# Kernel optimization log

Measured on AMD Instinct MI355X. Metric: run time of the kernel, lower is better.

Reference implementation:

```python
import jax, jax.numpy as jnp
import numpy as np

D = 1024
H = 8
DK = D // H
BS, NSEG, NSEN = 16, 64, 32


def _linear_params(key, d_in, d_out, scale=0.02):
    kw, kb = jax.random.split(key)
    w = jax.random.normal(kw, (d_out, d_in), dtype=jnp.float32) * scale
    b = jax.random.normal(kb, (d_out,), dtype=jnp.float32) * scale
    return w, b


def setup_inputs() -> dict:
    key = jax.random.key(0)
    ks = jax.random.split(key, 12)
    A = jax.random.normal(ks[0], (BS, NSEG, D), dtype=jnp.float32)
    V = jax.random.normal(ks[1], (BS, NSEG, D), dtype=jnp.float32)
    S = jax.random.normal(ks[2], (BS, NSEN, D), dtype=jnp.float32)
    wA, bA = _linear_params(ks[3], D, D)
    wV, bV = _linear_params(ks[4], D, D)
    wS, bS = _linear_params(ks[5], D, D)
    wq, bq = _linear_params(ks[6], D, D)
    wk, bk = _linear_params(ks[7], D, D)
    wv, bv = _linear_params(ks[8], D, D)
    w1, b1 = _linear_params(ks[9], D, D)
    w2, b2 = _linear_params(ks[10], D, D)
    return {"A": A, "V": V, "S": S,
            "wA": wA, "bA": bA, "wV": wV, "bV": bV, "wS": wS, "bS": bS,
            "wq": wq, "bq": bq, "wk": wk, "bk": bk, "wv": wv, "bv": bv,
            "w1": w1, "b1": b1, "w2": w2, "b2": b2}


def _lin(x, w, b):
    return x @ w.T + b


def reference(A, V, S, wA, bA, wV, bV, wS, bS, wq, bq, wk, bk, wv, bv, w1, b1, w2, b2):
    bs, num_seg, d_model = A.shape
    num_sen = S.shape[1]
    A = _lin(A, wA, bA)
    V = _lin(V, wV, bV)
    S = _lin(S, wS, bS)
    av = jnp.stack([A, V], axis=2)                       # (bs, num_seg, 2, d)
    q = _lin(S, wq, bq).reshape(bs, num_sen, H, DK)      # (b, s, h, dk)
    k = _lin(av, wk, bk).reshape(bs, num_seg, 2, H, DK)  # (b, g, a, h, dk)
    v = _lin(av, wv, bv).reshape(bs, num_seg, 2, H, DK)
    # attention over the size-2 A/V axis only
    attn = jnp.einsum('bshd,bgahd->bsgah', q, k) / np.sqrt(DK).astype(np.float32)
    attn = jax.nn.softmax(attn, axis=3)                  # softmax over a (A vs V)
    out = jnp.einsum('bsgah,bgahd->bsghd', attn, v)
    out = out.reshape(bs, num_sen, num_seg, d_model)
    # positionwise FF: Linear -> ReLU -> Linear (dropout p=0)
    out = _lin(jax.nn.relu(_lin(out, w1, b1)), w2, b2)
    return out
```

## Files before the change

### kernel.cpp

```cpp
#include <hip/hip_runtime.h>
#include <stdint.h>


#define D_MODEL 1024
#define N_HEAD  8
#define DK      128
#define BS      16
#define NSEG    64
#define NSEN    32

typedef __attribute__((ext_vector_type(8))) __bf16 bf16x8;
typedef __attribute__((ext_vector_type(8))) unsigned short u16x8;
typedef __attribute__((ext_vector_type(4))) float f32x4;

__device__ __forceinline__ float bf2f(unsigned short b) {
  union { unsigned int u; float f; } x; x.u = ((unsigned int)b) << 16; return x.f;
}
__device__ __forceinline__ unsigned short f2bf(float f) {
  union { float f; unsigned int u; } x; x.f = f;
  unsigned int u = x.u;
  unsigned int r = (u + 0x7fffu + ((u >> 16) & 1u)) >> 16;
  return (unsigned short)r;
}

__device__ __forceinline__ void g2l16(const void* g, void* l) {
  __builtin_amdgcn_global_load_lds(
      (const __attribute__((address_space(1))) void*)g,
      (__attribute__((address_space(3))) void*)l, 16, 0, 0);
}

struct CvtB { const float* s[11]; unsigned short* d[11]; int n4[11]; };
__global__ __launch_bounds__(256)
void cvtall_kernel(CvtB p) {
  const int z = blockIdx.y;
  const int i = blockIdx.x * 256 + threadIdx.x;
  if (i >= p.n4[z]) return;
  float4 v = reinterpret_cast<const float4*>(p.s[z])[i];
  ushort4 o;
  o.x = f2bf(v.x); o.y = f2bf(v.y); o.z = f2bf(v.z); o.w = f2bf(v.w);
  reinterpret_cast<ushort4*>(p.d[z])[i] = o;
}

struct GSeg { const unsigned short* A; const unsigned short* B;
              const float* bias; unsigned short* C; };
struct GBatch { GSeg s[3]; int end[3]; };

__global__ __launch_bounds__(256)
void gemm64_bt(GBatch gb) {
  __shared__ __align__(16) unsigned short lA[2][64 * 32];
  __shared__ __align__(16) unsigned short lB[2][128 * 32];

  const int nwg = gridDim.x;
  const int sw = (blockIdx.x & 7) * (nwg >> 3) + (blockIdx.x >> 3);
  int sgi = 0, base = 0;
  if (sw >= gb.end[0]) { sgi = 1; base = gb.end[0]; }
  if (sw >= gb.end[1]) { sgi = 2; base = gb.end[1]; }
  const GSeg sg = gb.s[sgi];
  const int st = sw - base;
  const int m0 = (st >> 3) * 64, n0 = (st & 7) * 128;

  const int t = threadIdx.x;
  const int lane = t & 63, w = t >> 6;
  const int fr = lane & 15, kg = lane >> 4;

  f32x4 acc[2][4] = {};

  const int r  = t >> 2;
  const int c8 = (t & 3) * 8;
  const unsigned short* ga  = sg.A + (size_t)(m0 + r) * 1024 + c8;
  const unsigned short* gbp = sg.B + (size_t)(n0 + r) * 1024 + c8;

  auto stage = [&](int buf, int k0) {
    g2l16(ga + k0,              &lA[buf][t * 8]);
    g2l16(gbp + k0,             &lB[buf][t * 8]);
    g2l16(gbp + k0 + 64 * 1024, &lB[buf][2048 + t * 8]);
  };

  stage(0, 0);
  asm volatile("s_waitcnt vmcnt(0)" ::: "memory");
  __syncthreads();

  for (int k0 = 0; k0 < 1024; k0 += 32) {
    const int buf = (k0 >> 5) & 1;
    if (k0 + 32 < 1024) stage(buf ^ 1, k0 + 32);

    u16x8 af[4], bf[2];
#pragma unroll
    for (int mi = 0; mi < 4; ++mi)
      af[mi] = *reinterpret_cast<const u16x8*>(&lA[buf][(mi * 16 + fr) * 32 + kg * 8]);
#pragma unroll
    for (int ni = 0; ni < 2; ++ni)
      bf[ni] = *reinterpret_cast<const u16x8*>(&lB[buf][(w * 32 + ni * 16 + fr) * 32 + kg * 8]);
#pragma unroll
    for (int ni = 0; ni < 2; ++ni)
#pragma unroll
      for (int mi = 0; mi < 4; ++mi)
        acc[ni][mi] = __builtin_amdgcn_mfma_f32_16x16x32_bf16(
            __builtin_bit_cast(bf16x8, bf[ni]), __builtin_bit_cast(bf16x8, af[mi]),
            acc[ni][mi], 0, 0, 0);

    asm volatile("s_waitcnt vmcnt(0)" ::: "memory");
    __syncthreads();
  }

#pragma unroll
  for (int ni = 0; ni < 2; ++ni) {
    const int gn0 = n0 + w * 32 + ni * 16 + kg * 4;
    const float4 bv = *reinterpret_cast<const float4*>(&sg.bias[gn0]);
#pragma unroll
    for (int mi = 0; mi < 4; ++mi) {
      const int gm = m0 + mi * 16 + fr;
      ushort4 o;
      o.x = f2bf(acc[ni][mi][0] + bv.x);
      o.y = f2bf(acc[ni][mi][1] + bv.y);
      o.z = f2bf(acc[ni][mi][2] + bv.z);
      o.w = f2bf(acc[ni][mi][3] + bv.w);
      *reinterpret_cast<ushort4*>(&sg.C[(size_t)gm * 1024 + gn0]) = o;
    }
  }
}

__global__ __launch_bounds__(512, 2)
void gemm8p_bt(const unsigned short* __restrict__ A, const unsigned short* __restrict__ B,
               const float* __restrict__ bias, float* __restrict__ C,
               int M, int N, int K, int nbx) {
  __shared__ __align__(16) unsigned short lds[2][2][256][64];

  const int nwg = gridDim.x;
  const int sw = (blockIdx.x & 7) * (nwg >> 3) + (blockIdx.x >> 3);
  const int m0 = (sw / nbx) * 256, n0 = (sw % nbx) * 256;

  const int T = threadIdx.x;
  const int lane = T & 63, wave = T >> 6;
  const int wr = wave >> 2, wc = wave & 3;
  const int fr = lane & 15, kg = lane >> 4;
  const int NT = K >> 6;

  const int sgs = (T & 7) ^ ((T >> 3) & 7);
  int grA[2][2], grB[2][2];
#pragma unroll
  for (int mh = 0; mh < 2; ++mh)
#pragma unroll
    for (int c = 0; c < 2; ++c) {
      int l = mh * 128 + c * 64 + (T >> 3);
      grA[mh][c] = ((l >> 6) & 1) * 128 + (l >> 7) * 64 + (l & 63);
      grB[mh][c] = ((l >> 5) & 3) * 64  + (l >> 7) * 32 + (l & 31);
    }
  const unsigned short* Abase = A + (size_t)m0 * K + sgs * 8;
  const unsigned short* Bbase = B + (size_t)n0 * K + sgs * 8;
  char* ldsc = (char*)&lds[0][0][0][0];

  auto stageA = [&](int buf, int mh, int t) {
#pragma unroll
    for (int c = 0; c < 2; ++c)
      g2l16(Abase + (size_t)grA[mh][c] * K + t * 64,
            ldsc + ((size_t)buf * 65536) + (mh * 128 + c * 64) * 128 + T * 16);
  };
  auto stageB = [&](int buf, int nh, int t) {
#pragma unroll
    for (int c = 0; c < 2; ++c)
      g2l16(Bbase + (size_t)grB[nh][c] * K + t * 64,
            ldsc + ((size_t)buf * 65536) + 32768 + (nh * 128 + c * 64) * 128 + T * 16);
  };

  int koff[2];
#pragma unroll
  for (int kk = 0; kk < 2; ++kk) koff[kk] = ((kk * 4 + kg) ^ (fr & 7)) * 16;
  int lrA[8], lrB[4];
#pragma unroll
  for (int mi = 0; mi < 8; ++mi) lrA[mi] = ((mi >> 2) * 128 + wr * 64 + (mi & 3) * 16 + fr) * 128;
#pragma unroll
  for (int ni = 0; ni < 4; ++ni) lrB[ni] = ((ni >> 1) * 128 + wc * 32 + (ni & 1) * 16 + fr) * 128;

  auto rdA = [&](int buf, int mi, int kk) -> u16x8 {
    return *reinterpret_cast<const u16x8*>(ldsc + (size_t)buf * 65536 + lrA[mi] + koff[kk]);
  };
  auto rdB = [&](int buf, int ni, int kk) -> u16x8 {
    return *reinterpret_cast<const u16x8*>(ldsc + (size_t)buf * 65536 + 32768 + lrB[ni] + koff[kk]);
  };

  f32x4 acc[4][8] = {};

  stageA(0, 0, 0); stageB(0, 0, 0); stageA(0, 1, 0); stageB(0, 1, 0);
  if (NT > 1) { stageA(1, 0, 1); stageB(1, 0, 1); stageA(1, 1, 1); }
  asm volatile("s_waitcnt vmcnt(6)" ::: "memory");
  __builtin_amdgcn_s_barrier();

  u16x8 af0[4][2], af1[4][2], bf0[2][2], bf1[2][2];

  for (int t = 0; t < NT; ++t) {
    const int buf = t & 1;
    const bool st1 = (t + 1 < NT), st2 = (t + 2 < NT);

#pragma unroll
    for (int mi = 0; mi < 4; ++mi)
#pragma unroll
      for (int kk = 0; kk < 2; ++kk) af0[mi][kk] = rdA(buf, mi, kk);
#pragma unroll
    for (int ni = 0; ni < 2; ++ni)
#pragma unroll
      for (int kk = 0; kk < 2; ++kk) bf0[ni][kk] = rdB(buf, ni, kk);
    if (st1) stageB(buf ^ 1, 1, t + 1);
    __builtin_amdgcn_s_barrier();
    asm volatile("s_waitcnt lgkmcnt(0)" ::: "memory");
    __builtin_amdgcn_sched_barrier(0);
    __builtin_amdgcn_s_setprio(1);
#pragma unroll
    for (int ni = 0; ni < 2; ++ni)
#pragma unroll
      for (int mi = 0; mi < 4; ++mi)
#pragma unroll
        for (int kk = 0; kk < 2; ++kk)
          acc[ni][mi] = __builtin_amdgcn_mfma_f32_16x16x32_bf16(
              __builtin_bit_cast(bf16x8, bf0[ni][kk]), __builtin_bit_cast(bf16x8, af0[mi][kk]),
              acc[ni][mi], 0, 0, 0);
    __builtin_amdgcn_s_setprio(0);
    __builtin_amdgcn_s_barrier();

#pragma unroll
    for (int ni = 0; ni < 2; ++ni)
#pragma unroll
      for (int kk = 0; kk < 2; ++kk) bf1[ni][kk] = rdB(buf, ni + 2, kk);
    if (st2) stageA(buf, 0, t + 2);
    __builtin_amdgcn_s_barrier();
    asm volatile("s_waitcnt lgkmcnt(0)" ::: "memory");
    __builtin_amdgcn_sched_barrier(0);
    __builtin_amdgcn_s_setprio(1);
#pragma unroll
    for (int ni = 0; ni < 2; ++ni)
#pragma unroll
      for (int mi = 0; mi < 4; ++mi)
#pragma unroll
        for (int kk = 0; kk < 2; ++kk)
          acc[ni + 2][mi] = __builtin_amdgcn_mfma_f32_16x16x32_bf16(
              __builtin_bit_cast(bf16x8, bf1[ni][kk]), __builtin_bit_cast(bf16x8, af0[mi][kk]),
              acc[ni + 2][mi], 0, 0, 0);
    __builtin_amdgcn_s_setprio(0);
    __builtin_amdgcn_s_barrier();

#pragma unroll
    for (int mi = 0; mi < 4; ++mi)
#pragma unroll
      for (int kk = 0; kk < 2; ++kk) af1[mi][kk] = rdA(buf, mi + 4, kk);
    if (st2) stageB(buf, 0, t + 2);
    __builtin_amdgcn_s_barrier();
    asm volatile("s_waitcnt lgkmcnt(0)" ::: "memory");
    __builtin_amdgcn_sched_barrier(0);
    __builtin_amdgcn_s_setprio(1);
#pragma unroll
    for (int ni = 0; ni < 2; ++ni)
#pragma unroll
      for (int mi = 0; mi < 4; ++mi)
#pragma unroll
        for (int kk = 0; kk < 2; ++kk)
          acc[ni + 2][mi + 4] = __builtin_amdgcn_mfma_f32_16x16x32_bf16(
              __builtin_bit_cast(bf16x8, bf1[ni][kk]), __builtin_bit_cast(bf16x8, af1[mi][kk]),
              acc[ni + 2][mi + 4], 0, 0, 0);
    __builtin_amdgcn_s_setprio(0);
    __builtin_amdgcn_s_barrier();

    if (st2) stageA(buf, 1, t + 2);
    __builtin_amdgcn_s_barrier();
    __builtin_amdgcn_s_setprio(1);
#pragma unroll
    for (int ni = 0; ni < 2; ++ni)
#pragma unroll
      for (int mi = 0; mi < 4; ++mi)
#pragma unroll
        for (int kk = 0; kk < 2; ++kk)
          acc[ni][mi + 4] = __builtin_amdgcn_mfma_f32_16x16x32_bf16(
              __builtin_bit_cast(bf16x8, bf0[ni][kk]), __builtin_bit_cast(bf16x8, af1[mi][kk]),
              acc[ni][mi + 4], 0, 0, 0);
    __builtin_amdgcn_s_setprio(0);
    if (st2)       asm volatile("s_waitcnt vmcnt(6)" ::: "memory");
    else if (st1)  asm volatile("s_waitcnt vmcnt(0)" ::: "memory");
    __builtin_amdgcn_s_barrier();
  }

#pragma unroll
  for (int ni = 0; ni < 4; ++ni) {
    const int gn0 = n0 + wc * 64 + ni * 16 + kg * 4;
    const float4 bv = *reinterpret_cast<const float4*>(&bias[gn0]);
#pragma unroll
    for (int mi = 0; mi < 8; ++mi) {
      const int gm = m0 + wr * 128 + mi * 16 + fr;
      float4 o;
      o.x = acc[ni][mi][0] + bv.x;
      o.y = acc[ni][mi][1] + bv.y;
      o.z = acc[ni][mi][2] + bv.z;
      o.w = acc[ni][mi][3] + bv.w;
      *reinterpret_cast<float4*>(&C[(size_t)gm * N + gn0]) = o;
    }
  }
}

__global__ __launch_bounds__(256)
void uav_gemm(const unsigned short* __restrict__ vAV, const unsigned short* __restrict__ w1,
              unsigned short* __restrict__ UAV) {
  __shared__ __align__(16) unsigned short lA[2][128 * 32];
  __shared__ __align__(16) unsigned short lB[2][128 * 32];

  const int zb = blockIdx.z;
  const int tensor = zb >> 3, h = zb & 7;
  const unsigned short* Ab = vAV + (size_t)tensor * (1024 * 1024) + h * 128;
  const unsigned short* Bb = w1 + h * 128;
  unsigned short* Cb = UAV + (size_t)tensor * (1024 * 8192) + h * 1024;

  const int t = threadIdx.x;
  const int m0 = blockIdx.y * 128, n0 = blockIdx.x * 128;
  const int lane = t & 63, wv = t >> 6;
  const int wrow = (wv >> 1) * 64, wcol = (wv & 1) * 64;
  const int fr = lane & 15, kg = lane >> 4;

  f32x4 acc[4][4] = {};

  const int r  = t >> 2;
  const int c8 = (t & 3) * 8;
  const unsigned short* ga = Ab + (size_t)(m0 + r) * 1024 + c8;
  const unsigned short* gb = Bb + (size_t)(n0 + r) * 1024 + c8;

  auto stage = [&](int buf, int k0) {
    g2l16(ga + k0,             &lA[buf][t * 8]);
    g2l16(ga + k0 + 64 * 1024, &lA[buf][2048 + t * 8]);
    g2l16(gb + k0,             &lB[buf][t * 8]);
    g2l16(gb + k0 + 64 * 1024, &lB[buf][2048 + t * 8]);
  };

  stage(0, 0);
  asm volatile("s_waitcnt vmcnt(0)" ::: "memory");
  __syncthreads();

  for (int k0 = 0; k0 < 128; k0 += 32) {
    const int buf = (k0 >> 5) & 1;
    if (k0 + 32 < 128) stage(buf ^ 1, k0 + 32);

    u16x8 af[4], bg_[4];
#pragma unroll
    for (int mi = 0; mi < 4; ++mi)
      af[mi] = *reinterpret_cast<const u16x8*>(&lA[buf][(wrow + mi * 16 + fr) * 32 + kg * 8]);
#pragma unroll
    for (int ni = 0; ni < 4; ++ni)
      bg_[ni] = *reinterpret_cast<const u16x8*>(&lB[buf][(wcol + ni * 16 + fr) * 32 + kg * 8]);
#pragma unroll
    for (int ni = 0; ni < 4; ++ni)
#pragma unroll
      for (int mi = 0; mi < 4; ++mi)
        acc[ni][mi] = __builtin_amdgcn_mfma_f32_16x16x32_bf16(
            __builtin_bit_cast(bf16x8, bg_[ni]), __builtin_bit_cast(bf16x8, af[mi]),
            acc[ni][mi], 0, 0, 0);

    asm volatile("s_waitcnt vmcnt(0)" ::: "memory");
    __syncthreads();
  }

#pragma unroll
  for (int ni = 0; ni < 4; ++ni) {
    const int gn0 = n0 + wcol + ni * 16 + kg * 4;
#pragma unroll
    for (int mi = 0; mi < 4; ++mi) {
      const int gm = m0 + wrow + mi * 16 + fr;
      ushort4 o;
      o.x = f2bf(acc[ni][mi][0]);
      o.y = f2bf(acc[ni][mi][1]);
      o.z = f2bf(acc[ni][mi][2]);
      o.w = f2bf(acc[ni][mi][3]);
      *reinterpret_cast<ushort4*>(&Cb[(size_t)gm * 8192 + gn0]) = o;
    }
  }
}

__global__ __launch_bounds__(256)
void score_hid_kernel(const unsigned short* __restrict__ q,
                      const unsigned short* __restrict__ kAV,
                      const unsigned short* __restrict__ UAV,
                      const float* __restrict__ b1,
                      unsigned short* __restrict__ hid) {
  const int bg = blockIdx.x;
  const int b = bg >> 6, g = bg & 63;
  __shared__ float sk[2][D_MODEL];
  __shared__ float pAl[NSEN][N_HEAD];
  const size_t rowA = (size_t)bg * D_MODEL;
  const size_t rowV = rowA + (size_t)BS * NSEG * D_MODEL;
  for (int i = threadIdx.x; i < D_MODEL; i += 256) {
    sk[0][i] = bf2f(kAV[rowA + i]);
    sk[1][i] = bf2f(kAV[rowV + i]);
  }
  __syncthreads();

  const int h = threadIdx.x >> 5;
  const int l = threadIdx.x & 31;
  const float scale = 0.08838834764831845f;

  for (int s = 0; s < NSEN; ++s) {
    const unsigned short* pq = q + ((size_t)(b * NSEN + s)) * D_MODEL + h * DK;
    float la = 0.f, lv = 0.f;
#pragma unroll
    for (int e = 0; e < 4; ++e) {
      int d = l + e * 32;
      float qv = bf2f(pq[d]);
      la += qv * sk[0][h * DK + d];
      lv += qv * sk[1][h * DK + d];
    }
#pragma unroll
    for (int off = 16; off; off >>= 1) {
      la += __shfl_xor(la, off, 32);
      lv += __shfl_xor(lv, off, 32);
    }
    if (l == 0) pAl[s][h] = 1.f / (1.f + __expf((lv - la) * scale));
  }
  __syncthreads();

  const int n0 = threadIdx.x * 4;
  const unsigned short* ua = UAV + (size_t)bg * 8192 + n0;
  const unsigned short* uv = ua + (size_t)1024 * 8192;

  float dU[N_HEAD][4];
  float base[4];
#pragma unroll
  for (int j = 0; j < 4; ++j) base[j] = b1[n0 + j];
#pragma unroll
  for (int hh = 0; hh < N_HEAD; ++hh) {
    ushort4 a4 = *reinterpret_cast<const ushort4*>(ua + hh * 1024);
    ushort4 v4 = *reinterpret_cast<const ushort4*>(uv + hh * 1024);
    float va[4] = {bf2f(a4.x), bf2f(a4.y), bf2f(a4.z), bf2f(a4.w)};
    float vv[4] = {bf2f(v4.x), bf2f(v4.y), bf2f(v4.z), bf2f(v4.w)};
#pragma unroll
    for (int j = 0; j < 4; ++j) { dU[hh][j] = va[j] - vv[j]; base[j] += vv[j]; }
  }

  for (int s = 0; s < NSEN; ++s) {
    float val[4] = {base[0], base[1], base[2], base[3]};
#pragma unroll
    for (int hh = 0; hh < N_HEAD; ++hh) {
      const float p = pAl[s][hh];
#pragma unroll
      for (int j = 0; j < 4; ++j) val[j] = fmaf(p, dU[hh][j], val[j]);
    }
    ushort4 o;
    o.x = f2bf(val[0] > 0.f ? val[0] : 0.f);
    o.y = f2bf(val[1] > 0.f ? val[1] : 0.f);
    o.z = f2bf(val[2] > 0.f ? val[2] : 0.f);
    o.w = f2bf(val[3] > 0.f ? val[3] : 0.f);
    size_t orow = ((size_t)(b * NSEN + s) * NSEG + g) * D_MODEL + n0;
    *reinterpret_cast<ushort4*>(hid + orow) = o;
  }
}

extern "C" void kernel_launch(void* const* d_in, const int* in_sizes, int n_in,
                              void* d_out, int out_size, void* d_ws, size_t ws_size,
                              hipStream_t stream) {
  const float* A  = (const float*)d_in[0];
  const float* V  = (const float*)d_in[1];
  const float* S  = (const float*)d_in[2];
  const float* wA = (const float*)d_in[3];  const float* bA = (const float*)d_in[4];
  const float* wV = (const float*)d_in[5];  const float* bV = (const float*)d_in[6];
  const float* wS = (const float*)d_in[7];  const float* bS = (const float*)d_in[8];
  const float* wq = (const float*)d_in[9];  const float* bq = (const float*)d_in[10];
  const float* wk = (const float*)d_in[11]; const float* bk = (const float*)d_in[12];
  const float* wv = (const float*)d_in[13]; const float* bv = (const float*)d_in[14];
  const float* w1 = (const float*)d_in[15]; const float* b1 = (const float*)d_in[16];
  const float* w2 = (const float*)d_in[17]; const float* b2 = (const float*)d_in[18];

  const int nAV = BS * NSEG * D_MODEL;
  const int nS  = BS * NSEN * D_MODEL;
  const int nW  = D_MODEL * D_MODEL;
  const int nCT = BS * NSEN * NSEG * D_MODEL;
  const int nU  = 2 * 1024 * 8 * 1024;

  char* ws = (char*)d_ws;
  size_t off = 0;
  auto carve = [&](size_t elems) {
    unsigned short* p = (unsigned short*)(ws + off);
    off += elems * sizeof(unsigned short);
    return p;
  };
  unsigned short* bwA = carve(nW);
  unsigned short* bwV = carve(nW);
  unsigned short* bwS = carve(nW);
  unsigned short* bwq = carve(nW);
  unsigned short* bwk = carve(nW);
  unsigned short* bwv = carve(nW);
  unsigned short* bw1 = carve(nW);
  unsigned short* bw2 = carve(nW);
  unsigned short* xA  = carve(nAV);
  unsigned short* xV  = carve(nAV);
  unsigned short* xS  = carve(nS);
  unsigned short* A1V1 = carve(2 * nAV);
  unsigned short* S1  = carve(nS);
  unsigned short* qb  = carve(nS);
  unsigned short* kAV = carve(2 * nAV);
  unsigned short* vAV = carve(2 * nAV);
  unsigned short* UAV = carve(nU);
  unsigned short* hid = carve(nCT);
  (void)ws_size; (void)n_in; (void)in_sizes; (void)out_size;

  CvtB cv;
  cv.s[0] = wA; cv.d[0] = bwA; cv.n4[0] = nW / 4;
  cv.s[1] = wV; cv.d[1] = bwV; cv.n4[1] = nW / 4;
  cv.s[2] = wS; cv.d[2] = bwS; cv.n4[2] = nW / 4;
  cv.s[3] = wq; cv.d[3] = bwq; cv.n4[3] = nW / 4;
  cv.s[4] = wk; cv.d[4] = bwk; cv.n4[4] = nW / 4;
  cv.s[5] = wv; cv.d[5] = bwv; cv.n4[5] = nW / 4;
  cv.s[6] = w1; cv.d[6] = bw1; cv.n4[6] = nW / 4;
  cv.s[7] = w2; cv.d[7] = bw2; cv.n4[7] = nW / 4;
  cv.s[8] = A;  cv.d[8] = xA;  cv.n4[8] = nAV / 4;
  cv.s[9] = V;  cv.d[9] = xV;  cv.n4[9] = nAV / 4;
  cv.s[10] = S; cv.d[10] = xS; cv.n4[10] = nS / 4;
  cvtall_kernel<<<dim3(1024, 11), dim3(256), 0, stream>>>(cv);

  GBatch pj;
  pj.s[0] = {xA, bwA, bA, A1V1};        pj.end[0] = 128;
  pj.s[1] = {xV, bwV, bV, A1V1 + nAV};  pj.end[1] = 256;
  pj.s[2] = {xS, bwS, bS, S1};          pj.end[2] = 320;
  gemm64_bt<<<dim3(320), 256, 0, stream>>>(pj);

  GBatch qkv;
  qkv.s[0] = {S1,   bwq, bq, qb};   qkv.end[0] = 64;
  qkv.s[1] = {A1V1, bwk, bk, kAV};  qkv.end[1] = 320;
  qkv.s[2] = {A1V1, bwv, bv, vAV};  qkv.end[2] = 576;
  gemm64_bt<<<dim3(576), 256, 0, stream>>>(qkv);

  uav_gemm<<<dim3(8, 8, 16), dim3(256), 0, stream>>>(vAV, bw1, UAV);

  score_hid_kernel<<<dim3(BS * NSEG), dim3(256), 0, stream>>>(qb, kAV, UAV, b1, hid);

  gemm8p_bt<<<dim3(512), 512, 0, stream>>>(hid, bw2, b2, (float*)d_out,
                                           32768, 1024, 1024, 4);
}
```

Before: 204.5 us.

## Replace 256x256 8-phase FF2 GEMM with simpler 256x128 tile double-buffered kernel

The final FF2 GEMM drops the 256x256-tile, 8-phase interleaved schedule (K-step 64) and uses a 256x128 tile with K-step 32 and plain double buffering, one barrier per iteration. LDS use falls from 128 KB to 48 KB per block, so more blocks can be resident (launch bounds raised to 4), and the grid doubles to 1024 blocks. In exchange each block gets less operand reuse and synchronises more often per unit of K, and loads are no longer overlapped as finely with MFMA work.

```diff
diff --git a/kernel.cpp b/kernel.cpp
--- a/kernel.cpp
+++ b/kernel.cpp
@@ -120,160 +120,80 @@
   }
 }
 
-__global__ __launch_bounds__(512, 2)
-void gemm8p_bt(const unsigned short* __restrict__ A, const unsigned short* __restrict__ B,
-               const float* __restrict__ bias, float* __restrict__ C,
-               int M, int N, int K, int nbx) {
-  __shared__ __align__(16) unsigned short lds[2][2][256][64];
+__global__ __launch_bounds__(512, 4)
+void ff2_gemm(const unsigned short* __restrict__ A, const unsigned short* __restrict__ B,
+              const float* __restrict__ bias, float* __restrict__ C,
+              int M, int N, int K) {
+  __shared__ __align__(16) unsigned short lds[2 * 12288];
 
   const int nwg = gridDim.x;
   const int sw = (blockIdx.x & 7) * (nwg >> 3) + (blockIdx.x >> 3);
-  const int m0 = (sw / nbx) * 256, n0 = (sw % nbx) * 256;
+  const int m0 = (sw >> 3) * 256, n0 = (sw & 7) * 128;
 
   const int T = threadIdx.x;
   const int lane = T & 63, wave = T >> 6;
-  const int wr = wave >> 2, wc = wave & 3;
+  const int wr = wave >> 1, wc = wave & 1;
   const int fr = lane & 15, kg = lane >> 4;
-  const int NT = K >> 6;
-
-  const int sgs = (T & 7) ^ ((T >> 3) & 7);
-  int grA[2][2], grB[2][2];
-#pragma unroll
-  for (int mh = 0; mh < 2; ++mh)
-#pragma unroll
-    for (int c = 0; c < 2; ++c) {
-      int l = mh * 128 + c * 64 + (T >> 3);
-      grA[mh][c] = ((l >> 6) & 1) * 128 + (l >> 7) * 64 + (l & 63);
-      grB[mh][c] = ((l >> 5) & 3) * 64  + (l >> 7) * 32 + (l & 31);
-    }
-  const unsigned short* Abase = A + (size_t)m0 * K + sgs * 8;
-  const unsigned short* Bbase = B + (size_t)n0 * K + sgs * 8;
-  char* ldsc = (char*)&lds[0][0][0][0];
-
-  auto stageA = [&](int buf, int mh, int t) {
-#pragma unroll
-    for (int c = 0; c < 2; ++c)
-      g2l16(Abase + (size_t)grA[mh][c] * K + t * 64,
-            ldsc + ((size_t)buf * 65536) + (mh * 128 + c * 64) * 128 + T * 16);
+  const int NT = K >> 5;
+
+  char* ldsc = (char*)lds;
+
+  const int srow = T >> 2;
+  const int gsl = ((T & 3) ^ ((srow & 3) ^ ((srow >> 2) & 3))) * 8;
+  const unsigned short* A0 = A + (size_t)(m0 + srow) * K + gsl;
+  const unsigned short* A1 = A + (size_t)(m0 + 128 + srow) * K + gsl;
+  const unsigned short* B0 = B + (size_t)(n0 + srow) * K + gsl;
+
+  auto stage = [&](int buf, int t) {
+    const int kb = t * 32;
+    char* dst = ldsc + buf * 24576 + T * 16;
+    g2l16(A0 + kb, dst);
+    g2l16(A1 + kb, dst + 8192);
+    g2l16(B0 + kb, dst + 16384);
   };
-  auto stageB = [&](int buf, int nh, int t) {
-#pragma unroll
-    for (int c = 0; c < 2; ++c)
-      g2l16(Bbase + (size_t)grB[nh][c] * K + t * 64,
-            ldsc + ((size_t)buf * 65536) + 32768 + (nh * 128 + c * 64) * 128 + T * 16);
-  };
-
-  int koff[2];
-#pragma unroll
-  for (int kk = 0; kk < 2; ++kk) koff[kk] = ((kk * 4 + kg) ^ (fr & 7)) * 16;
-  int lrA[8], lrB[4];
-#pragma unroll
-  for (int mi = 0; mi < 8; ++mi) lrA[mi] = ((mi >> 2) * 128 + wr * 64 + (mi & 3) * 16 + fr) * 128;
-#pragma unroll
-  for (int ni = 0; ni < 4; ++ni) lrB[ni] = ((ni >> 1) * 128 + wc * 32 + (ni & 1) * 16 + fr) * 128;
-
-  auto rdA = [&](int buf, int mi, int kk) -> u16x8 {
-    return *reinterpret_cast<const u16x8*>(ldsc + (size_t)buf * 65536 + lrA[mi] + koff[kk]);
-  };
-  auto rdB = [&](int buf, int ni, int kk) -> u16x8 {
-    return *reinterpret_cast<const u16x8*>(ldsc + (size_t)buf * 65536 + 32768 + lrB[ni] + koff[kk]);
-  };
-
-  f32x4 acc[4][8] = {};
-
-  stageA(0, 0, 0); stageB(0, 0, 0); stageA(0, 1, 0); stageB(0, 1, 0);
-  if (NT > 1) { stageA(1, 0, 1); stageB(1, 0, 1); stageA(1, 1, 1); }
-  asm volatile("s_waitcnt vmcnt(6)" ::: "memory");
+
+  int raddr[4], baddr[4];
+#pragma unroll
+  for (int mi = 0; mi < 4; ++mi) {
+    int lr = wr * 64 + mi * 16 + fr;
+    raddr[mi] = lr * 64 + ((kg ^ ((lr & 3) ^ ((lr >> 2) & 3))) * 16);
+  }
+#pragma unroll
+  for (int ni = 0; ni < 4; ++ni) {
+    int lr = wc * 64 + ni * 16 + fr;
+    baddr[ni] = 16384 + lr * 64 + ((kg ^ ((lr & 3) ^ ((lr >> 2) & 3))) * 16);
+  }
+
+  f32x4 acc[4][4] = {};
+
+  stage(0, 0);
+  asm volatile("s_waitcnt vmcnt(0)" ::: "memory");
   __builtin_amdgcn_s_barrier();
-
-  u16x8 af0[4][2], af1[4][2], bf0[2][2], bf1[2][2];
 
   for (int t = 0; t < NT; ++t) {
     const int buf = t & 1;
-    const bool st1 = (t + 1 < NT), st2 = (t + 2 < NT);
-
+    if (t + 1 < NT) stage(buf ^ 1, t + 1);
+
+    const char* base = ldsc + buf * 24576;
+    u16x8 af[4], bf[4];
 #pragma unroll
     for (int mi = 0; mi < 4; ++mi)
-#pragma unroll
-      for (int kk = 0; kk < 2; ++kk) af0[mi][kk] = rdA(buf, mi, kk);
-#pragma unroll
-    for (int ni = 0; ni < 2; ++ni)
-#pragma unroll
-      for (int kk = 0; kk < 2; ++kk) bf0[ni][kk] = rdB(buf, ni, kk);
-    if (st1) stageB(buf ^ 1, 1, t + 1);
-    __builtin_amdgcn_s_barrier();
-    asm volatile("s_waitcnt lgkmcnt(0)" ::: "memory");
-    __builtin_amdgcn_sched_barrier(0);
+      af[mi] = *reinterpret_cast<const u16x8*>(base + raddr[mi]);
+#pragma unroll
+    for (int ni = 0; ni < 4; ++ni)
+      bf[ni] = *reinterpret_cast<const u16x8*>(base + baddr[ni]);
+
     __builtin_amdgcn_s_setprio(1);
 #pragma unroll
-    for (int ni = 0; ni < 2; ++ni)
+    for (int ni = 0; ni < 4; ++ni)
 #pragma unroll
       for (int mi = 0; mi < 4; ++mi)
-#pragma unroll
-        for (int kk = 0; kk < 2; ++kk)
-          acc[ni][mi] = __builtin_amdgcn_mfma_f32_16x16x32_bf16(
-              __builtin_bit_cast(bf16x8, bf0[ni][kk]), __builtin_bit_cast(bf16x8, af0[mi][kk]),
-              acc[ni][mi], 0, 0, 0);
+        acc[ni][mi] = __builtin_amdgcn_mfma_f32_16x16x32_bf16(
+            __builtin_bit_cast(bf16x8, bf[ni]), __builtin_bit_cast(bf16x8, af[mi]),
+            acc[ni][mi], 0, 0, 0);
     __builtin_amdgcn_s_setprio(0);
-    __builtin_amdgcn_s_barrier();
-
-#pragma unroll
-    for (int ni = 0; ni < 2; ++ni)
-#pragma unroll
-      for (int kk = 0; kk < 2; ++kk) bf1[ni][kk] = rdB(buf, ni + 2, kk);
-    if (st2) stageA(buf, 0, t + 2);
-    __builtin_amdgcn_s_barrier();
-    asm volatile("s_waitcnt lgkmcnt(0)" ::: "memory");
-    __builtin_amdgcn_sched_barrier(0);
-    __builtin_amdgcn_s_setprio(1);
-#pragma unroll
-    for (int ni = 0; ni < 2; ++ni)
-#pragma unroll
-      for (int mi = 0; mi < 4; ++mi)
-#pragma unroll
-        for (int kk = 0; kk < 2; ++kk)
-          acc[ni + 2][mi] = __builtin_amdgcn_mfma_f32_16x16x32_bf16(
-              __builtin_bit_cast(bf16x8, bf1[ni][kk]), __builtin_bit_cast(bf16x8, af0[mi][kk]),
-              acc[ni + 2][mi], 0, 0, 0);
-    __builtin_amdgcn_s_setprio(0);
-    __builtin_amdgcn_s_barrier();
-
-#pragma unroll
-    for (int mi = 0; mi < 4; ++mi)
-#pragma unroll
-      for (int kk = 0; kk < 2; ++kk) af1[mi][kk] = rdA(buf, mi + 4, kk);
-    if (st2) stageB(buf, 0, t + 2);
-    __builtin_amdgcn_s_barrier();
-    asm volatile("s_waitcnt lgkmcnt(0)" ::: "memory");
-    __builtin_amdgcn_sched_barrier(0);
-    __builtin_amdgcn_s_setprio(1);
-#pragma unroll
-    for (int ni = 0; ni < 2; ++ni)
-#pragma unroll
-      for (int mi = 0; mi < 4; ++mi)
-#pragma unroll
-        for (int kk = 0; kk < 2; ++kk)
-          acc[ni + 2][mi + 4] = __builtin_amdgcn_mfma_f32_16x16x32_bf16(
-              __builtin_bit_cast(bf16x8, bf1[ni][kk]), __builtin_bit_cast(bf16x8, af1[mi][kk]),
-              acc[ni + 2][mi + 4], 0, 0, 0);
-    __builtin_amdgcn_s_setprio(0);
-    __builtin_amdgcn_s_barrier();
-
-    if (st2) stageA(buf, 1, t + 2);
-    __builtin_amdgcn_s_barrier();
-    __builtin_amdgcn_s_setprio(1);
-#pragma unroll
-    for (int ni = 0; ni < 2; ++ni)
-#pragma unroll
-      for (int mi = 0; mi < 4; ++mi)
-#pragma unroll
-        for (int kk = 0; kk < 2; ++kk)
-          acc[ni][mi + 4] = __builtin_amdgcn_mfma_f32_16x16x32_bf16(
-              __builtin_bit_cast(bf16x8, bf0[ni][kk]), __builtin_bit_cast(bf16x8, af1[mi][kk]),
-              acc[ni][mi + 4], 0, 0, 0);
-    __builtin_amdgcn_s_setprio(0);
-    if (st2)       asm volatile("s_waitcnt vmcnt(6)" ::: "memory");
-    else if (st1)  asm volatile("s_waitcnt vmcnt(0)" ::: "memory");
+
+    asm volatile("s_waitcnt vmcnt(0)" ::: "memory");
     __builtin_amdgcn_s_barrier();
   }
 
@@ -282,8 +202,8 @@
     const int gn0 = n0 + wc * 64 + ni * 16 + kg * 4;
     const float4 bv = *reinterpret_cast<const float4*>(&bias[gn0]);
 #pragma unroll
-    for (int mi = 0; mi < 8; ++mi) {
-      const int gm = m0 + wr * 128 + mi * 16 + fr;
+    for (int mi = 0; mi < 4; ++mi) {
+      const int gm = m0 + wr * 64 + mi * 16 + fr;
       float4 o;
       o.x = acc[ni][mi][0] + bv.x;
       o.y = acc[ni][mi][1] + bv.y;
@@ -524,6 +444,6 @@
 
   score_hid_kernel<<<dim3(BS * NSEG), dim3(256), 0, stream>>>(qb, kAV, UAV, b1, hid);
 
-  gemm8p_bt<<<dim3(512), 512, 0, stream>>>(hid, bw2, b2, (float*)d_out,
-                                           32768, 1024, 1024, 4);
-}
+  ff2_gemm<<<dim3(1024), 512, 0, stream>>>(hid, bw2, b2, (float*)d_out,
+                                           32768, 1024, 1024);
+}
```

New measurement: 211.2 us. 1.03x slower.
